# Optimization experiments

Measured on AMD Instinct MI355X. Metric: run time of the kernel, lower is better.

## Reference

```python
import jax, jax.numpy as jnp
import numpy as np

N, E, B, DIM, NF, EF, HID = 16384, 32768, 512, 64, 14, 4, 128

def _p(key, shape, scale):
    return jax.random.normal(key, shape, dtype=jnp.float32) * scale

def setup_inputs() -> dict:
    key = jax.random.key(0)
    ks = jax.random.split(key, 20)
    s = lambda fan: 1.0 / float(np.sqrt(fan))
    z = lambda *sh: jnp.zeros(sh, jnp.float32)
    return {
        "x": jax.random.normal(ks[0], (N, NF), dtype=jnp.float32),
        "edge_index": jax.random.randint(ks[1], (2, E), 0, N),
        "edge_attr": jax.random.uniform(ks[2], (E, EF), dtype=jnp.float32),
        "batch": jnp.sort(jax.random.randint(ks[3], (N,), 0, B)),
        "do_dropout": 0,
        "mlp_drop": 0,
        "lin0_w": _p(ks[4], (NF, DIM), s(NF)), "lin0_b": z(DIM),
        "nn1_w": _p(ks[5], (EF, HID), s(EF)), "nn1_b": z(HID),
        "nn2_w": _p(ks[6], (HID, DIM * DIM), s(HID)), "nn2_b": z(DIM * DIM),
        "root_w": _p(ks[7], (DIM, DIM), s(DIM)), "conv_b": z(DIM),
        "gru_w_ih": _p(ks[8], (3 * DIM, DIM), s(DIM)), "gru_w_hh": _p(ks[9], (3 * DIM, DIM), s(DIM)),
        "gru_b_ih": _p(ks[10], (3 * DIM,), s(DIM)), "gru_b_hh": _p(ks[11], (3 * DIM,), s(DIM)),
        "lstm_w_ih": _p(ks[12], (4 * DIM, 2 * DIM), s(DIM)), "lstm_w_hh": _p(ks[13], (4 * DIM, DIM), s(DIM)),
        "lstm_b_ih": _p(ks[14], (4 * DIM,), s(DIM)), "lstm_b_hh": _p(ks[15], (4 * DIM,), s(DIM)),
        "lin1_w": _p(ks[16], (2 * DIM, DIM), s(2 * DIM)), "lin1_b": z(DIM),
        "lin2_w": _p(ks[17], (DIM, 1), s(DIM)), "lin2_b": z(1),
    }

def _forward(x, edge_attr, lin0_w, lin0_b, nn1_w, nn1_b, nn2_w, nn2_b, root_w, conv_b,
             gru_w_ih, gru_w_hh, gru_b_ih, gru_b_hh,
             lstm_w_ih, lstm_w_hh, lstm_b_ih, lstm_b_hh,
             lin1_w, lin1_b, lin2_w, lin2_b, edge_index, batch):
    src, dst = edge_index[0], edge_index[1]
    out = jax.nn.relu(x @ lin0_w + lin0_b)                      # [N, DIM]
    h = out
    # Edge-conditioned weights (edge_attr is layer-independent -> compute once)
    ew = jax.nn.relu(edge_attr @ nn1_w + nn1_b) @ nn2_w + nn2_b  # [E, DIM*DIM]
    ew = ew.reshape(E, DIM, DIM)
    deg = jax.ops.segment_sum(jnp.ones((E,), jnp.float32), dst, num_segments=N)
    deg = jnp.maximum(deg, 1.0)[:, None]                        # mean aggregation denominator

    def gru_cell(xin, hprev):
        gi = xin @ gru_w_ih.T + gru_b_ih
        gh = hprev @ gru_w_hh.T + gru_b_hh
        ir, iz, inn = jnp.split(gi, 3, axis=-1)
        hr, hz, hn = jnp.split(gh, 3, axis=-1)
        r = jax.nn.sigmoid(ir + hr)
        zg = jax.nn.sigmoid(iz + hz)
        n = jnp.tanh(inn + r * hn)
        return (1.0 - zg) * n + zg * hprev

    for _ in range(3):  # 3 message-passing rounds (structurally fixed)
        msg = jnp.einsum('ed,edf->ef', out[src], ew)            # gather -> per-edge matvec
        agg = jax.ops.segment_sum(msg, dst, num_segments=N) / deg
        m = jax.nn.relu(out @ root_w + agg + conv_b)            # NNConv (root weight + mean aggr)
        h = gru_cell(m, h)
        out = h

    # Set2Set pooling, 3 processing steps
    q_star = jnp.zeros((B, 2 * DIM), jnp.float32)
    hl = jnp.zeros((B, DIM), jnp.float32)
    cl = jnp.zeros((B, DIM), jnp.float32)
    for _ in range(3):
        gates = q_star @ lstm_w_ih.T + lstm_b_ih + hl @ lstm_w_hh.T + lstm_b_hh
        ii, ff, gg, oo = jnp.split(gates, 4, axis=-1)
        cl = jax.nn.sigmoid(ff) * cl + jax.nn.sigmoid(ii) * jnp.tanh(gg)
        hl = jax.nn.sigmoid(oo) * jnp.tanh(cl)
        q = hl                                                  # [B, DIM]
        e = jnp.sum(out * q[batch], axis=-1)                    # [N]
        emax = jax.ops.segment_max(e, batch, num_segments=B)
        ex = jnp.exp(e - emax[batch])
        esum = jnp.maximum(jax.ops.segment_sum(ex, batch, num_segments=B), 1e-16)
        a = ex / esum[batch]                                    # segment softmax
        r = jax.ops.segment_sum(a[:, None] * out, batch, num_segments=B)
        q_star = jnp.concatenate([q, r], axis=-1)               # [B, 2*DIM]

    y = jax.nn.relu(q_star @ lin1_w + lin1_b)
    # dropout flags are False (eval) -> identity
    y = y @ lin2_w + lin2_b
    return y.reshape(-1)                                        # [B]

def reference(x, edge_index, edge_attr, batch, do_dropout, mlp_drop,
              lin0_w, lin0_b, nn1_w, nn1_b, nn2_w, nn2_b, root_w, conv_b,
              gru_w_ih, gru_w_hh, gru_b_ih, gru_b_hh,
              lstm_w_ih, lstm_w_hh, lstm_b_ih, lstm_b_hh,
              lin1_w, lin1_b, lin2_w, lin2_b):
    return _forward(x, edge_attr, lin0_w, lin0_b, nn1_w, nn1_b, nn2_w, nn2_b, root_w, conv_b,
                    gru_w_ih, gru_w_hh, gru_b_ih, gru_b_hh,
                    lstm_w_ih, lstm_w_hh, lstm_b_ih, lstm_b_hh,
                    lin1_w, lin1_b, lin2_w, lin2_b, edge_index, batch)
```

## Files before the change

### kernel.cpp

```cpp
#include <hip/hip_runtime.h>
#include <math.h>

#define N_NODES 16384
#define N_EDGES 32768
#define NGRAPH  512
#define DIM     64
#define NF      14
#define HIDN    128
#define EWCOLS  4096

typedef unsigned short u16;
typedef unsigned int   u32;
typedef __attribute__((ext_vector_type(8))) short bf16x8;
typedef __attribute__((ext_vector_type(4))) float f32x4;
typedef __attribute__((ext_vector_type(4))) u32   u32x4;
typedef __attribute__((address_space(1))) const u32 as1_u32;
typedef __attribute__((address_space(3))) u32       as3_u32;

__device__ inline float b2f(u16 u){
    unsigned int x = ((unsigned int)u) << 16;
    return __builtin_bit_cast(float, x);
}
__device__ inline u16 f2b(float f){
    unsigned int x = __builtin_bit_cast(unsigned int, f);
    unsigned int r = (x + 0x7FFFu + ((x >> 16) & 1u)) >> 16;
    return (u16)r;
}
__device__ inline float sigf(float x){ return 1.f / (1.f + expf(-x)); }

__global__ __launch_bounds__(256) void k_lin0(const float* __restrict__ x,
        const float* __restrict__ w, const float* __restrict__ b, float* __restrict__ out){
    int n = (blockIdx.x * blockDim.x + threadIdx.x) >> 6;
    int lane = threadIdx.x & 63;
    if (n >= N_NODES) return;
    float xv = (lane < NF) ? x[n * NF + lane] : 0.f;
    float acc = b[lane];
    #pragma unroll
    for (int d = 0; d < NF; ++d){
        float xd = __shfl(xv, d);
        acc += xd * w[d * DIM + lane];
    }
    out[n * DIM + lane] = fmaxf(acc, 0.f);
}

__global__ __launch_bounds__(256) void k_prep(const float* __restrict__ w2,
        const float* __restrict__ lwih, const float* __restrict__ lwhh,
        const float* __restrict__ root, const float* __restrict__ gwih, const float* __restrict__ gwhh,
        u16* __restrict__ w2T, float* __restrict__ wihT, float* __restrict__ whhT,
        u16* __restrict__ rtHi, u16* __restrict__ rtLo,
        u16* __restrict__ wihHi, u16* __restrict__ wihLo,
        u16* __restrict__ whhHi, u16* __restrict__ whhLo){
    int i = blockIdx.x * 256 + threadIdx.x;
    if (i < 524288){
        int k = i >> 12, c = i & 4095;
        w2T[c * HIDN + k] = f2b(w2[i]);
    } else if (i < 557056){
        int i2 = i - 524288;
        int j = i2 >> 7, d = i2 & 127;
        wihT[d * 256 + j] = lwih[i2];
    } else if (i < 573440){
        int i2 = i - 557056;
        int j = i2 >> 6, d = i2 & 63;
        whhT[d * 256 + j] = lwhh[i2];
    } else if (i < 577536){
        int i2 = i - 573440;
        int d = i2 >> 6, j = i2 & 63;
        float v = root[i2]; u16 h = f2b(v);
        rtHi[j * 64 + d] = h; rtLo[j * 64 + d] = f2b(v - b2f(h));
    } else if (i < 589824){
        int k = i - 577536;
        float v = gwih[k]; u16 h = f2b(v);
        wihHi[k] = h; wihLo[k] = f2b(v - b2f(h));
    } else if (i < 602112){
        int k = i - 589824;
        float v = gwhh[k]; u16 h = f2b(v);
        whhHi[k] = h; whhLo[k] = f2b(v - b2f(h));
    }
}

__global__ __launch_bounds__(256) void k_deg(const int* __restrict__ ei, unsigned* __restrict__ degu){
    int e = blockIdx.x * blockDim.x + threadIdx.x;
    if (e < N_EDGES) atomicAdd(&degu[ei[N_EDGES + e]], 1u);
}
__global__ __launch_bounds__(256) void k_dinv(const unsigned* __restrict__ degu, float* __restrict__ dinv){
    int n = blockIdx.x * blockDim.x + threadIdx.x;
    if (n < N_NODES) dinv[n] = 1.f / fmaxf((float)degu[n], 1.f);
}

#define EB   128
#define LDT_O 132

__global__ __launch_bounds__(512) void k_msg_fused(
        const int* __restrict__ ei, const float* __restrict__ ea,
        const float* __restrict__ w1, const float* __restrict__ b1,
        const u16* __restrict__ w2T, const float* __restrict__ b2,
        const float* __restrict__ out, float* __restrict__ agg)
{
    __shared__ float s_oT[64 * LDT_O];
    __shared__ u16   s_b[2][64 * 128];
    __shared__ float s_w1[512];
    __shared__ float s_b1[128];
    int tid = threadIdx.x;
    int e0 = blockIdx.x * EB;
    int wv = tid >> 6, lane = tid & 63;

    int c0 = (wv*2)     * 4 + (lane >> 4);
    int c1 = (wv*2 + 1) * 4 + (lane >> 4);
    int o0 = ((((lane & 15) << 4) ^ ((c0 & 7) << 4)) >> 1);
    int o1 = ((((lane & 15) << 4) ^ ((c1 & 7) << 4)) >> 1);
    const u16* g0 = w2T + c0 * HIDN + o0;
    const u16* g1 = w2T + c1 * HIDN + o1;

    __builtin_amdgcn_global_load_lds((as1_u32*)g0,
        (as3_u32*)((char*)s_b[0] + (wv*2)*1024), 16, 0, 0);
    __builtin_amdgcn_global_load_lds((as1_u32*)g1,
        (as3_u32*)((char*)s_b[0] + (wv*2+1)*1024), 16, 0, 0);

    s_w1[tid] = w1[tid];
    if (tid < 128) s_b1[tid] = b1[tid];
    {
        int row = tid >> 2, q = tid & 3;
        int s = ei[e0 + row];
        const float4* sp = (const float4*)(out + (size_t)s * DIM + q * 16);
        float4 v0 = sp[0], v1 = sp[1], v2 = sp[2], v3 = sp[3];
        float* op = s_oT + (q * 16) * LDT_O + row;
        op[0*LDT_O]=v0.x;  op[1*LDT_O]=v0.y;  op[2*LDT_O]=v0.z;  op[3*LDT_O]=v0.w;
        op[4*LDT_O]=v1.x;  op[5*LDT_O]=v1.y;  op[6*LDT_O]=v1.z;  op[7*LDT_O]=v1.w;
        op[8*LDT_O]=v2.x;  op[9*LDT_O]=v2.y;  op[10*LDT_O]=v2.z; op[11*LDT_O]=v2.w;
        op[12*LDT_O]=v3.x; op[13*LDT_O]=v3.y; op[14*LDT_O]=v3.z; op[15*LDT_O]=v3.w;
    }
    __syncthreads();

    int WR = (wv >> 1) * 32, WC = (wv & 1) * 32;
    int lr = lane & 15, lk = (lane >> 4) * 8;
    int crow = (lane >> 4) * 4;
    int swzr = (lr & 7) << 4;

    bf16x8 afr[2][4];
    #pragma unroll
    for (int m = 0; m < 2; ++m){
        int erow = e0 + WR + m*16 + lr;
        float4 av = *(const float4*)(ea + (size_t)erow * 4);
        #pragma unroll
        for (int kk = 0; kk < 4; ++kk){
            bf16x8 t8;
            #pragma unroll
            for (int i = 0; i < 8; ++i){
                int h = kk*32 + lk + i;
                float acc = s_b1[h] + av.x*s_w1[h] + av.y*s_w1[128+h]
                          + av.z*s_w1[256+h] + av.w*s_w1[384+h];
                t8[i] = (short)f2b(fmaxf(acc, 0.f));
            }
            afr[m][kk] = t8;
        }
    }

    f32x4 msg[2][2] = {};

    for (int d = 0; d < 64; ++d){
        if (d + 1 < 64){
            size_t pb = (size_t)(d + 1) * 8192;
            char* dst = (char*)s_b[(d + 1) & 1];
            __builtin_amdgcn_global_load_lds((as1_u32*)(g0 + pb),
                (as3_u32*)(dst + (wv*2)*1024), 16, 0, 0);
            __builtin_amdgcn_global_load_lds((as1_u32*)(g1 + pb),
                (as3_u32*)(dst + (wv*2+1)*1024), 16, 0, 0);
        }
        const char* sr = (const char*)s_b[d & 1];
        f32x4 ew00 = {}, ew01 = {}, ew10 = {}, ew11 = {};
        #pragma unroll
        for (int kk = 0; kk < 4; ++kk){
            int kb = kk*64 + (lane >> 4) * 16;
            bf16x8 bf0 = *(const bf16x8*)(sr + (((WC + lr)*256 + kb)      ^ swzr));
            bf16x8 bf1 = *(const bf16x8*)(sr + (((WC + 16 + lr)*256 + kb) ^ swzr));
            ew00 = __builtin_amdgcn_mfma_f32_16x16x32_bf16(afr[0][kk], bf0, ew00, 0, 0, 0);
            ew01 = __builtin_amdgcn_mfma_f32_16x16x32_bf16(afr[0][kk], bf1, ew01, 0, 0, 0);
            ew10 = __builtin_amdgcn_mfma_f32_16x16x32_bf16(afr[1][kk], bf0, ew10, 0, 0, 0);
            ew11 = __builtin_amdgcn_mfma_f32_16x16x32_bf16(afr[1][kk], bf1, ew11, 0, 0, 0);
        }
        f32x4 sc0 = *(const f32x4*)(s_oT + d * LDT_O + WR + crow);
        f32x4 sc1 = *(const f32x4*)(s_oT + d * LDT_O + WR + 16 + crow);
        #pragma unroll
        for (int r = 0; r < 4; ++r){
            msg[0][0][r] += sc0[r] * ew00[r];
            msg[0][1][r] += sc0[r] * ew01[r];
            msg[1][0][r] += sc1[r] * ew10[r];
            msg[1][1][r] += sc1[r] * ew11[r];
        }
        __syncthreads();
    }

    int f0 = WC + lr;
    #pragma unroll 8
    for (int dd = 0; dd < 64; ++dd){
        float bv0 = b2[dd*64 + f0];
        float bv1 = b2[dd*64 + f0 + 16];
        f32x4 sc0 = *(const f32x4*)(s_oT + dd * LDT_O + WR + crow);
        f32x4 sc1 = *(const f32x4*)(s_oT + dd * LDT_O + WR + 16 + crow);
        #pragma unroll
        for (int r = 0; r < 4; ++r){
            msg[0][0][r] += sc0[r] * bv0;
            msg[0][1][r] += sc0[r] * bv1;
            msg[1][0][r] += sc1[r] * bv0;
            msg[1][1][r] += sc1[r] * bv1;
        }
    }

    #pragma unroll
    for (int m = 0; m < 2; ++m){
        #pragma unroll
        for (int r = 0; r < 4; ++r){
            int eg = e0 + WR + m*16 + crow + r;
            int dn = ei[N_EDGES + eg];
            atomicAdd(&agg[(size_t)dn * DIM + WC + lr],      msg[m][0][r]);
            atomicAdd(&agg[(size_t)dn * DIM + WC + 16 + lr], msg[m][1][r]);
        }
    }
}

#define LDH 68
__global__ __launch_bounds__(256) void k_update(
        const u16* __restrict__ rtHi, const u16* __restrict__ rtLo,
        const u16* __restrict__ wihHi, const u16* __restrict__ wihLo,
        const u16* __restrict__ whhHi, const u16* __restrict__ whhLo,
        const float* __restrict__ convb, const float* __restrict__ bih,
        const float* __restrict__ bhh,
        const float* __restrict__ agg, const float* __restrict__ dinv,
        float* __restrict__ out)
{
    __shared__ float s_h[64 * LDH];
    __shared__ float s_aux[64 * LDH];
    __shared__ float s_m[64 * LDH];
    int tid = threadIdx.x;
    int n0 = blockIdx.x * 64;

    {
        int row = tid >> 2, cb = (tid & 3) * 16;
        const float4* hp = (const float4*)(out + (size_t)(n0 + row) * DIM + cb);
        const float4* ap = (const float4*)(agg + (size_t)(n0 + row) * DIM + cb);
        float di = dinv[n0 + row];
        #pragma unroll
        for (int q = 0; q < 4; ++q){
            float4 hv = hp[q];
            float4 av = ap[q];
            *(float4*)(s_h + row * LDH + cb + q*4) = hv;
            float4 xv;
            xv.x = av.x * di + convb[cb + q*4 + 0];
            xv.y = av.y * di + convb[cb + q*4 + 1];
            xv.z = av.z * di + convb[cb + q*4 + 2];
            xv.w = av.w * di + convb[cb + q*4 + 3];
            *(float4*)(s_aux + row * LDH + cb + q*4) = xv;
        }
    }
    __syncthreads();

    int wv = tid >> 6, lane = tid & 63;
    int lr = lane & 15, lkb = (lane >> 4) * 8;
    int arow = wv * 16 + lr;

    bf16x8 hHi[2], hLo[2];
    #pragma unroll
    for (int kk = 0; kk < 2; ++kk){
        const float* src = s_h + arow * LDH + kk*32 + lkb;
        bf16x8 hi8, lo8;
        #pragma unroll
        for (int e = 0; e < 8; ++e){
            float v = src[e];
            u16 h = f2b(v);
            hi8[e] = (short)h;
            lo8[e] = (short)f2b(v - b2f(h));
        }
        hHi[kk] = hi8; hLo[kk] = lo8;
    }

    f32x4 c1[4] = {};
    #pragma unroll
    for (int ct = 0; ct < 4; ++ct){
        #pragma unroll
        for (int kk = 0; kk < 2; ++kk){
            int off = (ct*16 + lr) * 64 + kk*32 + lkb;
            bf16x8 bHi = *(const bf16x8*)(rtHi + off);
            bf16x8 bLo = *(const bf16x8*)(rtLo + off);
            c1[ct] = __builtin_amdgcn_mfma_f32_16x16x32_bf16(hHi[kk], bHi, c1[ct], 0, 0, 0);
            c1[ct] = __builtin_amdgcn_mfma_f32_16x16x32_bf16(hLo[kk], bHi, c1[ct], 0, 0, 0);
            c1[ct] = __builtin_amdgcn_mfma_f32_16x16x32_bf16(hHi[kk], bLo, c1[ct], 0, 0, 0);
        }
    }

    int crow = (lane >> 4) * 4;
    #pragma unroll
    for (int ct = 0; ct < 4; ++ct){
        #pragma unroll
        for (int r = 0; r < 4; ++r){
            int row = wv*16 + crow + r;
            int col = ct*16 + lr;
            float m = fmaxf(c1[ct][r] + s_aux[row * LDH + col], 0.f);
            s_m[row * LDH + col] = m;
        }
    }
    __syncthreads();

    bf16x8 mHi[2], mLo[2];
    #pragma unroll
    for (int kk = 0; kk < 2; ++kk){
        const float* src = s_m + arow * LDH + kk*32 + lkb;
        bf16x8 hi8, lo8;
        #pragma unroll
        for (int e = 0; e < 8; ++e){
            float v = src[e];
            u16 h = f2b(v);
            hi8[e] = (short)h;
            lo8[e] = (short)f2b(v - b2f(h));
        }
        mHi[kk] = hi8; mLo[kk] = lo8;
    }

    f32x4 gi[12] = {}, gh[12] = {};
    #pragma unroll
    for (int ct = 0; ct < 12; ++ct){
        #pragma unroll
        for (int kk = 0; kk < 2; ++kk){
            int off = (ct*16 + lr) * 64 + kk*32 + lkb;
            bf16x8 biH = *(const bf16x8*)(wihHi + off);
            bf16x8 biL = *(const bf16x8*)(wihLo + off);
            gi[ct] = __builtin_amdgcn_mfma_f32_16x16x32_bf16(mHi[kk], biH, gi[ct], 0, 0, 0);
            gi[ct] = __builtin_amdgcn_mfma_f32_16x16x32_bf16(mLo[kk], biH, gi[ct], 0, 0, 0);
            gi[ct] = __builtin_amdgcn_mfma_f32_16x16x32_bf16(mHi[kk], biL, gi[ct], 0, 0, 0);
            bf16x8 bhH = *(const bf16x8*)(whhHi + off);
            bf16x8 bhL = *(const bf16x8*)(whhLo + off);
            gh[ct] = __builtin_amdgcn_mfma_f32_16x16x32_bf16(hHi[kk], bhH, gh[ct], 0, 0, 0);
            gh[ct] = __builtin_amdgcn_mfma_f32_16x16x32_bf16(hLo[kk], bhH, gh[ct], 0, 0, 0);
            gh[ct] = __builtin_amdgcn_mfma_f32_16x16x32_bf16(hHi[kk], bhL, gh[ct], 0, 0, 0);
        }
    }

    #pragma unroll
    for (int ct = 0; ct < 4; ++ct){
        int col = ct*16 + lr;
        float br_i = bih[col],       br_h = bhh[col];
        float bz_i = bih[64 + col],  bz_h = bhh[64 + col];
        float bn_i = bih[128 + col], bn_h = bhh[128 + col];
        #pragma unroll
        for (int r = 0; r < 4; ++r){
            int row = wv*16 + crow + r;
            float rg = sigf(gi[ct][r] + br_i + gh[ct][r] + br_h);
            float zg = sigf(gi[ct+4][r] + bz_i + gh[ct+4][r] + bz_h);
            float ng = tanhf(gi[ct+8][r] + bn_i + rg * (gh[ct+8][r] + bn_h));
            float h  = s_h[row * LDH + col];
            s_aux[row * LDH + col] = (1.f - zg) * ng + zg * h;
        }
    }
    __syncthreads();

    {
        int row = tid >> 2, cb = (tid & 3) * 16;
        #pragma unroll
        for (int q = 0; q < 4; ++q)
            *(float4*)(out + (size_t)(n0 + row) * DIM + cb + q*4) =
                *(const float4*)(s_aux + row * LDH + cb + q*4);
    }
}

__global__ __launch_bounds__(256) void k_s2s(
        const float* __restrict__ out, const int* __restrict__ batch,
        const float* __restrict__ wihT, const float* __restrict__ lbih,
        const float* __restrict__ whhT, const float* __restrict__ lbhh,
        const float* __restrict__ l1w, const float* __restrict__ l1b,
        const float* __restrict__ l2w, const float* __restrict__ l2b,
        float* __restrict__ y)
{
    __shared__ float s_q[128];
    __shared__ float s_hc[128];
    __shared__ float s_g[256];
    __shared__ float s_rw[256];
    __shared__ float s_sw[8];
    __shared__ int   s_rng[2];
    int g = blockIdx.x, tid = threadIdx.x;
    if (tid < 2){
        int target = g + tid;
        int lo = 0, hi = N_NODES;
        while (lo < hi){ int mid = (lo + hi) >> 1; if (batch[mid] < target) lo = mid + 1; else hi = mid; }
        s_rng[tid] = lo;
    }
    if (tid < 128){ s_q[tid] = 0.f; s_hc[tid] = 0.f; }
    __syncthreads();
    int s0 = s_rng[0], s1 = s_rng[1];
    int wv = tid >> 6, lane = tid & 63;

    for (int step = 0; step < 3; ++step){
        float acc = lbih[tid] + lbhh[tid];
        #pragma unroll 8
        for (int d = 0; d < 128; ++d) acc += s_q[d] * wihT[d * 256 + tid];
        #pragma unroll 8
        for (int d = 0; d < 64;  ++d) acc += s_hc[d] * whhT[d * 256 + tid];
        s_g[tid] = acc;
        __syncthreads();
        if (tid < 64){
            float c = sigf(s_g[64 + tid]) * s_hc[64 + tid] + sigf(s_g[tid]) * tanhf(s_g[128 + tid]);
            float h = sigf(s_g[192 + tid]) * tanhf(c);
            s_hc[tid] = h; s_hc[64 + tid] = c;
            s_q[tid] = h;
        }
        __syncthreads();
        float q = s_hc[lane];
        float emx = -3.4e38f;
        for (int n = s0 + wv; n < s1; n += 4){
            float v = out[(size_t)n * DIM + lane] * q;
            #pragma unroll
            for (int off = 32; off; off >>= 1) v += __shfl_xor(v, off);
            emx = fmaxf(emx, v);
        }
        if (lane == 0) s_sw[wv] = emx;
        __syncthreads();
        float gmax = fmaxf(fmaxf(s_sw[0], s_sw[1]), fmaxf(s_sw[2], s_sw[3]));
        float rl = 0.f, ss = 0.f;
        for (int n = s0 + wv; n < s1; n += 4){
            float o = out[(size_t)n * DIM + lane];
            float v = o * q;
            #pragma unroll
            for (int off = 32; off; off >>= 1) v += __shfl_xor(v, off);
            float ex = expf(v - gmax);
            rl += ex * o;
            ss += ex;
        }
        s_rw[wv * 64 + lane] = rl;
        if (lane == 0) s_sw[4 + wv] = ss;
        __syncthreads();
        if (tid < 64){
            float r = s_rw[tid] + s_rw[64 + tid] + s_rw[128 + tid] + s_rw[192 + tid];
            float S = fmaxf(s_sw[4] + s_sw[5] + s_sw[6] + s_sw[7], 1e-16f);
            s_q[64 + tid] = r / S;
        }
        __syncthreads();
    }
    if (wv == 0){
        float acc = l1b[lane];
        #pragma unroll 8
        for (int d = 0; d < 128; ++d) acc += s_q[d] * l1w[d * 64 + lane];
        float h = fmaxf(acc, 0.f);
        float p = h * l2w[lane];
        #pragma unroll
        for (int off = 32; off; off >>= 1) p += __shfl_down(p, off);
        if (lane == 0) y[g] = p + l2b[0];
    }
}

extern "C" void kernel_launch(void* const* d_in, const int* in_sizes, int n_in,
                              void* d_out, int out_size, void* d_ws, size_t ws_size,
                              hipStream_t stream){
    const float* x      = (const float*)d_in[0];
    const int*   ei     = (const int*)d_in[1];
    const float* ea     = (const float*)d_in[2];
    const int*   batch  = (const int*)d_in[3];
    const float* lin0_w = (const float*)d_in[6];
    const float* lin0_b = (const float*)d_in[7];
    const float* nn1_w  = (const float*)d_in[8];
    const float* nn1_b  = (const float*)d_in[9];
    const float* nn2_w  = (const float*)d_in[10];
    const float* nn2_b  = (const float*)d_in[11];
    const float* root_w = (const float*)d_in[12];
    const float* conv_b = (const float*)d_in[13];
    const float* gwih   = (const float*)d_in[14];
    const float* gwhh   = (const float*)d_in[15];
    const float* gbih   = (const float*)d_in[16];
    const float* gbhh   = (const float*)d_in[17];
    const float* lwih   = (const float*)d_in[18];
    const float* lwhh   = (const float*)d_in[19];
    const float* lbih   = (const float*)d_in[20];
    const float* lbhh   = (const float*)d_in[21];
    const float* l1w    = (const float*)d_in[22];
    const float* l1b    = (const float*)d_in[23];
    const float* l2w    = (const float*)d_in[24];
    const float* l2b    = (const float*)d_in[25];
    float* y = (float*)d_out;

    char* p = (char*)d_ws;
    float* out   = (float*)p;    p += (size_t)N_NODES * DIM * 4;
    float* agg   = (float*)p;    p += (size_t)N_NODES * DIM * 4;
    u16* w2T     = (u16*)p;      p += (size_t)EWCOLS * HIDN * 2;
    float* wihT  = (float*)p;    p += 128 * 256 * 4;
    float* whhT  = (float*)p;    p += 64 * 256 * 4;
    u16* rtHi    = (u16*)p;      p += 4096 * 2;
    u16* rtLo    = (u16*)p;      p += 4096 * 2;
    u16* wihHi   = (u16*)p;      p += 12288 * 2;
    u16* wihLo   = (u16*)p;      p += 12288 * 2;
    u16* whhHi   = (u16*)p;      p += 12288 * 2;
    u16* whhLo   = (u16*)p;      p += 12288 * 2;
    unsigned* degu = (unsigned*)p; p += N_NODES * 4;
    float* dinv  = (float*)p;    p += N_NODES * 4;

    if ((size_t)(p - (char*)d_ws) > ws_size) return;

    hipMemsetAsync(degu, 0, N_NODES * 4, stream);

    k_prep<<<2352, 256, 0, stream>>>(nn2_w, lwih, lwhh, root_w, gwih, gwhh,
                w2T, wihT, whhT, rtHi, rtLo, wihHi, wihLo, whhHi, whhLo);
    k_lin0<<<N_NODES / 4, 256, 0, stream>>>(x, lin0_w, lin0_b, out);
    k_deg <<<N_EDGES / 256, 256, 0, stream>>>(ei, degu);
    k_dinv<<<N_NODES / 256, 256, 0, stream>>>(degu, dinv);

    for (int r = 0; r < 3; ++r){
        hipMemsetAsync(agg, 0, (size_t)N_NODES * DIM * 4, stream);
        k_msg_fused<<<N_EDGES / EB, 512, 0, stream>>>(ei, ea, nn1_w, nn1_b, w2T, nn2_b, out, agg);
        k_update   <<<N_NODES / 64, 256, 0, stream>>>(rtHi, rtLo, wihHi, wihLo, whhHi, whhLo,
                        conv_b, gbih, gbhh, agg, dinv, out);
    }

    k_s2s<<<NGRAPH, 256, 0, stream>>>(out, batch, wihT, lbih, whhT, lbhh,
                l1w, l1b, l2w, l2b, y);
}
```

Before: 357.7 us.

## Pre-swizzle edge-weight matrix into MFMA fragment order and load directly to registers

Result: faster. 337.7 us (-5.6%).

```diff
diff --git a/kernel.cpp b/kernel.cpp
--- a/kernel.cpp
+++ b/kernel.cpp
@@ -13,9 +13,6 @@
 typedef unsigned int   u32;
 typedef __attribute__((ext_vector_type(8))) short bf16x8;
 typedef __attribute__((ext_vector_type(4))) float f32x4;
-typedef __attribute__((ext_vector_type(4))) u32   u32x4;
-typedef __attribute__((address_space(1))) const u32 as1_u32;
-typedef __attribute__((address_space(3))) u32       as3_u32;
 
 __device__ inline float b2f(u16 u){
     unsigned int x = ((unsigned int)u) << 16;
@@ -46,14 +43,17 @@
 __global__ __launch_bounds__(256) void k_prep(const float* __restrict__ w2,
         const float* __restrict__ lwih, const float* __restrict__ lwhh,
         const float* __restrict__ root, const float* __restrict__ gwih, const float* __restrict__ gwhh,
-        u16* __restrict__ w2T, float* __restrict__ wihT, float* __restrict__ whhT,
+        u16* __restrict__ w2F, float* __restrict__ wihT, float* __restrict__ whhT,
         u16* __restrict__ rtHi, u16* __restrict__ rtLo,
         u16* __restrict__ wihHi, u16* __restrict__ wihLo,
         u16* __restrict__ whhHi, u16* __restrict__ whhLo){
     int i = blockIdx.x * 256 + threadIdx.x;
     if (i < 524288){
         int k = i >> 12, c = i & 4095;
-        w2T[c * HIDN + k] = f2b(w2[i]);
+        int d = c >> 6, cg = (c >> 4) & 3, kk = k >> 5;
+        int lane = ((k >> 3) & 3) * 16 + (c & 15);
+        int elem = k & 7;
+        w2F[((((d*16 + cg*4 + kk) << 6) + lane) << 3) + elem] = f2b(w2[i]);
     } else if (i < 557056){
         int i2 = i - 524288;
         int j = i2 >> 7, d = i2 & 127;
@@ -90,31 +90,18 @@
 #define EB   128
 #define LDT_O 132
 
-__global__ __launch_bounds__(512) void k_msg_fused(
+__global__ __launch_bounds__(512, 2) void k_msg_fused(
         const int* __restrict__ ei, const float* __restrict__ ea,
         const float* __restrict__ w1, const float* __restrict__ b1,
-        const u16* __restrict__ w2T, const float* __restrict__ b2,
+        const u16* __restrict__ w2F, const float* __restrict__ b2,
         const float* __restrict__ out, float* __restrict__ agg)
 {
     __shared__ float s_oT[64 * LDT_O];
-    __shared__ u16   s_b[2][64 * 128];
     __shared__ float s_w1[512];
     __shared__ float s_b1[128];
     int tid = threadIdx.x;
     int e0 = blockIdx.x * EB;
     int wv = tid >> 6, lane = tid & 63;
-
-    int c0 = (wv*2)     * 4 + (lane >> 4);
-    int c1 = (wv*2 + 1) * 4 + (lane >> 4);
-    int o0 = ((((lane & 15) << 4) ^ ((c0 & 7) << 4)) >> 1);
-    int o1 = ((((lane & 15) << 4) ^ ((c1 & 7) << 4)) >> 1);
-    const u16* g0 = w2T + c0 * HIDN + o0;
-    const u16* g1 = w2T + c1 * HIDN + o1;
-
-    __builtin_amdgcn_global_load_lds((as1_u32*)g0,
-        (as3_u32*)((char*)s_b[0] + (wv*2)*1024), 16, 0, 0);
-    __builtin_amdgcn_global_load_lds((as1_u32*)g1,
-        (as3_u32*)((char*)s_b[0] + (wv*2+1)*1024), 16, 0, 0);
 
     s_w1[tid] = w1[tid];
     if (tid < 128) s_b1[tid] = b1[tid];
@@ -131,14 +118,16 @@
     }
     __syncthreads();
 
-    int WR = (wv >> 1) * 32, WC = (wv & 1) * 32;
+    int rg = wv >> 2;
+    int cg = wv & 3;
+    int WR = rg * 64;
+    int WCOL = cg * 16;
     int lr = lane & 15, lk = (lane >> 4) * 8;
     int crow = (lane >> 4) * 4;
-    int swzr = (lr & 7) << 4;
-
-    bf16x8 afr[2][4];
-    #pragma unroll
-    for (int m = 0; m < 2; ++m){
+
+    bf16x8 afr[4][4];
+    #pragma unroll
+    for (int m = 0; m < 4; ++m){
         int erow = e0 + WR + m*16 + lr;
         float4 av = *(const float4*)(ea + (size_t)erow * 4);
         #pragma unroll
@@ -155,65 +144,70 @@
         }
     }
 
-    f32x4 msg[2][2] = {};
-
-    for (int d = 0; d < 64; ++d){
-        if (d + 1 < 64){
-            size_t pb = (size_t)(d + 1) * 8192;
-            char* dst = (char*)s_b[(d + 1) & 1];
-            __builtin_amdgcn_global_load_lds((as1_u32*)(g0 + pb),
-                (as3_u32*)(dst + (wv*2)*1024), 16, 0, 0);
-            __builtin_amdgcn_global_load_lds((as1_u32*)(g1 + pb),
-                (as3_u32*)(dst + (wv*2+1)*1024), 16, 0, 0);
-        }
-        const char* sr = (const char*)s_b[d & 1];
-        f32x4 ew00 = {}, ew01 = {}, ew10 = {}, ew11 = {};
-        #pragma unroll
-        for (int kk = 0; kk < 4; ++kk){
-            int kb = kk*64 + (lane >> 4) * 16;
-            bf16x8 bf0 = *(const bf16x8*)(sr + (((WC + lr)*256 + kb)      ^ swzr));
-            bf16x8 bf1 = *(const bf16x8*)(sr + (((WC + 16 + lr)*256 + kb) ^ swzr));
-            ew00 = __builtin_amdgcn_mfma_f32_16x16x32_bf16(afr[0][kk], bf0, ew00, 0, 0, 0);
-            ew01 = __builtin_amdgcn_mfma_f32_16x16x32_bf16(afr[0][kk], bf1, ew01, 0, 0, 0);
-            ew10 = __builtin_amdgcn_mfma_f32_16x16x32_bf16(afr[1][kk], bf0, ew10, 0, 0, 0);
-            ew11 = __builtin_amdgcn_mfma_f32_16x16x32_bf16(afr[1][kk], bf1, ew11, 0, 0, 0);
-        }
-        f32x4 sc0 = *(const f32x4*)(s_oT + d * LDT_O + WR + crow);
-        f32x4 sc1 = *(const f32x4*)(s_oT + d * LDT_O + WR + 16 + crow);
-        #pragma unroll
-        for (int r = 0; r < 4; ++r){
-            msg[0][0][r] += sc0[r] * ew00[r];
-            msg[0][1][r] += sc0[r] * ew01[r];
-            msg[1][0][r] += sc1[r] * ew10[r];
-            msg[1][1][r] += sc1[r] * ew11[r];
-        }
-        __syncthreads();
-    }
-
-    int f0 = WC + lr;
+    const bf16x8* gw = (const bf16x8*)w2F;
+    f32x4 msg[4] = {};
+    bf16x8 bA[4], bB[4];
+
+#define LOADB(F, dd) { \
+    int base = (((dd)*16 + cg*4) << 6) + lane; \
+    F[0] = gw[base];       F[1] = gw[base + 64]; \
+    F[2] = gw[base + 128]; F[3] = gw[base + 192]; }
+
+#define COMPUTE(F, dd) { \
+    f32x4 ew0 = {}, ew1 = {}, ew2 = {}, ew3 = {}; \
+    _Pragma("unroll") \
+    for (int kk = 0; kk < 4; ++kk){ \
+        ew0 = __builtin_amdgcn_mfma_f32_16x16x32_bf16(afr[0][kk], F[kk], ew0, 0, 0, 0); \
+        ew1 = __builtin_amdgcn_mfma_f32_16x16x32_bf16(afr[1][kk], F[kk], ew1, 0, 0, 0); \
+        ew2 = __builtin_amdgcn_mfma_f32_16x16x32_bf16(afr[2][kk], F[kk], ew2, 0, 0, 0); \
+        ew3 = __builtin_amdgcn_mfma_f32_16x16x32_bf16(afr[3][kk], F[kk], ew3, 0, 0, 0); \
+    } \
+    f32x4 sc0 = *(const f32x4*)(s_oT + (dd) * LDT_O + WR + crow); \
+    f32x4 sc1 = *(const f32x4*)(s_oT + (dd) * LDT_O + WR + 16 + crow); \
+    f32x4 sc2 = *(const f32x4*)(s_oT + (dd) * LDT_O + WR + 32 + crow); \
+    f32x4 sc3 = *(const f32x4*)(s_oT + (dd) * LDT_O + WR + 48 + crow); \
+    _Pragma("unroll") \
+    for (int r = 0; r < 4; ++r){ \
+        msg[0][r] += sc0[r] * ew0[r]; \
+        msg[1][r] += sc1[r] * ew1[r]; \
+        msg[2][r] += sc2[r] * ew2[r]; \
+        msg[3][r] += sc3[r] * ew3[r]; \
+    } }
+
+    LOADB(bA, 0);
+    for (int d = 0; d < 64; d += 2){
+        LOADB(bB, d + 1);
+        COMPUTE(bA, d);
+        if (d + 2 < 64) LOADB(bA, d + 2);
+        COMPUTE(bB, d + 1);
+    }
+#undef LOADB
+#undef COMPUTE
+
+    int f0 = WCOL + lr;
     #pragma unroll 8
     for (int dd = 0; dd < 64; ++dd){
-        float bv0 = b2[dd*64 + f0];
-        float bv1 = b2[dd*64 + f0 + 16];
+        float bv = b2[dd*64 + f0];
         f32x4 sc0 = *(const f32x4*)(s_oT + dd * LDT_O + WR + crow);
         f32x4 sc1 = *(const f32x4*)(s_oT + dd * LDT_O + WR + 16 + crow);
+        f32x4 sc2 = *(const f32x4*)(s_oT + dd * LDT_O + WR + 32 + crow);
+        f32x4 sc3 = *(const f32x4*)(s_oT + dd * LDT_O + WR + 48 + crow);
         #pragma unroll
         for (int r = 0; r < 4; ++r){
-            msg[0][0][r] += sc0[r] * bv0;
-            msg[0][1][r] += sc0[r] * bv1;
-            msg[1][0][r] += sc1[r] * bv0;
-            msg[1][1][r] += sc1[r] * bv1;
-        }
-    }
-
-    #pragma unroll
-    for (int m = 0; m < 2; ++m){
+            msg[0][r] += sc0[r] * bv;
+            msg[1][r] += sc1[r] * bv;
+            msg[2][r] += sc2[r] * bv;
+            msg[3][r] += sc3[r] * bv;
+        }
+    }
+
+    #pragma unroll
+    for (int m = 0; m < 4; ++m){
         #pragma unroll
         for (int r = 0; r < 4; ++r){
             int eg = e0 + WR + m*16 + crow + r;
             int dn = ei[N_EDGES + eg];
-            atomicAdd(&agg[(size_t)dn * DIM + WC + lr],      msg[m][0][r]);
-            atomicAdd(&agg[(size_t)dn * DIM + WC + 16 + lr], msg[m][1][r]);
+            atomicAdd(&agg[(size_t)dn * DIM + WCOL + lr], msg[m][r]);
         }
     }
 }
@@ -477,7 +471,7 @@
     char* p = (char*)d_ws;
     float* out   = (float*)p;    p += (size_t)N_NODES * DIM * 4;
     float* agg   = (float*)p;    p += (size_t)N_NODES * DIM * 4;
-    u16* w2T     = (u16*)p;      p += (size_t)EWCOLS * HIDN * 2;
+    u16* w2F     = (u16*)p;      p += (size_t)EWCOLS * HIDN * 2;
     float* wihT  = (float*)p;    p += 128 * 256 * 4;
     float* whhT  = (float*)p;    p += 64 * 256 * 4;
     u16* rtHi    = (u16*)p;      p += 4096 * 2;
@@ -494,14 +488,14 @@
     hipMemsetAsync(degu, 0, N_NODES * 4, stream);
 
     k_prep<<<2352, 256, 0, stream>>>(nn2_w, lwih, lwhh, root_w, gwih, gwhh,
-                w2T, wihT, whhT, rtHi, rtLo, wihHi, wihLo, whhHi, whhLo);
+                w2F, wihT, whhT, rtHi, rtLo, wihHi, wihLo, whhHi, whhLo);
     k_lin0<<<N_NODES / 4, 256, 0, stream>>>(x, lin0_w, lin0_b, out);
     k_deg <<<N_EDGES / 256, 256, 0, stream>>>(ei, degu);
     k_dinv<<<N_NODES / 256, 256, 0, stream>>>(degu, dinv);
 
     for (int r = 0; r < 3; ++r){
         hipMemsetAsync(agg, 0, (size_t)N_NODES * DIM * 4, stream);
-        k_msg_fused<<<N_EDGES / EB, 512, 0, stream>>>(ei, ea, nn1_w, nn1_b, w2T, nn2_b, out, agg);
+        k_msg_fused<<<N_EDGES / EB, 512, 0, stream>>>(ei, ea, nn1_w, nn1_b, w2F, nn2_b, out, agg);
         k_update   <<<N_NODES / 64, 256, 0, stream>>>(rtHi, rtLo, wihHi, wihLo, whhHi, whhLo,
                         conv_b, gbih, gbhh, agg, dinv, out);
     }
```
